# Kernel optimization log

Hardware: AMD Instinct MI355X
Metric: run time of the kernel (lower is better)

Reference implementation:

```python
import jax, jax.numpy as jnp
import numpy as np

B, T_IN, T_OUT, N, C, H, K1 = 4, 12, 24, 5000, 32, 8, 17  # K1 = k+1 (self included)
SIGMA_RATIO = 2.0
BETA = 0.8  # Swish beta
W_THRESH = 1e-5


def setup_inputs() -> dict:
    key = jax.random.key(0)
    k1, k2, k3, k4, k5 = jax.random.split(key, 5)
    x = jax.random.normal(k1, (B, T_IN, N, C), jnp.float32)
    nearest_nodes = jax.random.randint(k2, (N, K1), 0, N)  # int indices; -1 allowed by module semantics
    nearest_dists = jax.random.uniform(k3, (N, K1), jnp.float32) * 100.0
    W_shrink = jax.random.normal(k4, (T_IN * H, T_OUT - T_IN), jnp.float32) / np.float32(np.sqrt(T_IN * H))
    b_shrink = jax.random.normal(k5, (T_OUT - T_IN,), jnp.float32) * 0.01
    return {"x": x, "nearest_nodes": nearest_nodes, "nearest_dists": nearest_dists,
            "W_shrink": W_shrink, "b_shrink": b_shrink}


def reference(x, nearest_nodes, nearest_dists, W_shrink, b_shrink):
    Bx, t, n, c = x.shape
    sigma = nearest_dists.max() / SIGMA_RATIO
    lam = jnp.arange(1, H + 1, dtype=jnp.float32) / H  # (H,)
    nd = nearest_dists.reshape(-1)                      # (N*K1,)
    nn = nearest_nodes.reshape(-1)                      # (N*K1,)
    # GCN weights: exp(-d^2 * lambda / sigma^2), zeroed for missing (-1) neighbors and tiny values
    w = jnp.exp(-(nd[:, None] ** 2) * lam / (sigma ** 2))  # (N*K1, H)
    w = jnp.where(nn[:, None] == -1, 0.0, w)
    w = jnp.where(w < W_THRESH, 0.0, w)
    # pad row so index -1 hits zeros (jax -1 wraps to last row, matching torch)
    pad_x = jnp.concatenate([x, jnp.zeros((Bx, t, 1, c), x.dtype)], axis=2)
    x_nb = pad_x[:, :, nn].reshape(Bx, t, n, K1, c)         # gathered neighbors (B,t,N,K1,C)
    w3 = w.reshape(n, K1, H)
    # fused gather-weight-sum over neighbor dim j -> (B,t,N,H,C)
    agg = jnp.einsum('btnjc,njh->btnhc', x_nb, w3)
    # (B,t,N,H,C) -> (B,N,C,t,H) -> (B,N,C,t*H)
    feat = agg.transpose(0, 2, 4, 1, 3).reshape(Bx, n, c, t * H)
    y = feat @ W_shrink + b_shrink                          # (B,N,C,T-t_in)
    y = y.transpose(0, 3, 1, 2)                             # (B,T-t_in,N,C)
    y = y * jax.nn.sigmoid(BETA * y)                        # Swish
    return jnp.concatenate([x, y], axis=1)                  # (B,T,N,C)
```

## Files before the change

kernel.cpp:

```cpp
#include <hip/hip_runtime.h>

#define BB     4
#define T_IN   12
#define T_OUT  24
#define NNODES 5000
#define CC     32
#define HH     8
#define K1     17
#define O_OUT  12
#define XSTRIDE (NNODES*CC)
#define TPU     (NNODES*16)

#define XB2_BN  192
#define XB2_B   (NNODES*XB2_BN)
#define JP      9
#define VJPD    36
#define VQD     (JP*VJPD)
#define VND     (4*VQD)
#define PREPB   938

__global__ void max_reduce_kernel(const float* __restrict__ d, int n,
                                  unsigned* __restrict__ out) {
    float m = 0.0f;
    for (int i = blockIdx.x * blockDim.x + threadIdx.x; i < n;
         i += gridDim.x * blockDim.x)
        m = fmaxf(m, d[i]);
#pragma unroll
    for (int off = 32; off > 0; off >>= 1)
        m = fmaxf(m, __shfl_down(m, off, 64));
    if ((threadIdx.x & 63) == 0)
        atomicMax(out, __float_as_uint(m));
}

__device__ inline unsigned bf16rne(float f) {
    unsigned u = __float_as_uint(f);
    return (u + 0x7FFFu + ((u >> 16) & 1u)) >> 16;
}

__global__ void fused_prep_kernel(const float4* __restrict__ x,
                                  float4* __restrict__ out,
                                  uint4* __restrict__ xb2,
                                  const int* __restrict__ nn,
                                  const float* __restrict__ nd,
                                  const float* __restrict__ Wsh,
                                  const unsigned* __restrict__ maxbits,
                                  unsigned* __restrict__ Vb2) {
    __shared__ float wjl[144];
    const int tid = threadIdx.x;

    if (blockIdx.x < PREPB) {
        const int total = BB * T_IN * NNODES;
        for (int i = blockIdx.x * blockDim.x + tid; i < total;
             i += PREPB * blockDim.x) {
            int bt = i / NNODES;
            int n  = i - bt * NNODES;
            int b  = bt / T_IN;
            int t  = bt - b * T_IN;
            const float4* xr = x + (size_t)i * 8;
            float4* orow = out + ((size_t)(b * T_OUT + t) * NNODES + n) * 8;
            uint4* xrow  = xb2 + ((size_t)(b * NNODES + n) * T_IN + t) * 4;
#pragma unroll
            for (int vq = 0; vq < 4; ++vq) {
                float4 v0 = xr[2 * vq], v1 = xr[2 * vq + 1];
                orow[2 * vq] = v0; orow[2 * vq + 1] = v1;
                uint4 pk;
                pk.x = bf16rne(v0.x) | (bf16rne(v0.y) << 16);
                pk.y = bf16rne(v0.z) | (bf16rne(v0.w) << 16);
                pk.z = bf16rne(v1.x) | (bf16rne(v1.y) << 16);
                pk.w = bf16rne(v1.z) | (bf16rne(v1.w) << 16);
                xrow[vq] = pk;
            }
        }
    } else {
        const int n = blockIdx.x - PREPB;
        if (tid < 144) {
            int j = tid >> 3, h = tid & 7;
            float wv = 0.f;
            if (j < K1) {
                float mx = __uint_as_float(*maxbits);
                float inv_s2 = 4.0f / (mx * mx);
                float dv = nd[n * K1 + j];
                float lam = (float)(h + 1) * 0.125f;
                wv = expf(-dv * dv * lam * inv_s2);
                if (nn[n * K1 + j] == -1 || wv < 1e-5f) wv = 0.0f;
            }
            wjl[tid] = wv;
        }
        __syncthreads();
        if (tid < 144) {
            const int t = tid / 12;
            const int o = tid - t * 12;
            float Wcol[8];
#pragma unroll
            for (int h = 0; h < 8; ++h) Wcol[h] = Wsh[(t * 8 + h) * 12 + o];
            unsigned* vn = Vb2 + (size_t)n * VND
                         + (t / 3) * VQD + (t % 3) * 12 + o;
#pragma unroll
            for (int jp = 0; jp < JP; ++jp) {
                float4 a0 = *(const float4*)&wjl[jp * 16];
                float4 a1 = *(const float4*)&wjl[jp * 16 + 4];
                float4 b0 = *(const float4*)&wjl[jp * 16 + 8];
                float4 b1 = *(const float4*)&wjl[jp * 16 + 12];
                float wa[8] = {a0.x, a0.y, a0.z, a0.w, a1.x, a1.y, a1.z, a1.w};
                float wb[8] = {b0.x, b0.y, b0.z, b0.w, b1.x, b1.y, b1.z, b1.w};
                float v0 = 0.f, v1 = 0.f;
#pragma unroll
                for (int h = 0; h < 8; ++h) {
                    v0 = fmaf(wa[h], Wcol[h], v0);
                    v1 = fmaf(wb[h], Wcol[h], v1);
                }
                vn[jp * VJPD] = bf16rne(v0) | (bf16rne(v1) << 16);
            }
        }
    }
}

struct VBlk { uint4 v[9]; };

__device__ __forceinline__ unsigned u4c(const uint4& u, int i) {
    switch (i) { case 0: return u.x; case 1: return u.y;
                 case 2: return u.z; default: return u.w; }
}

#define DOT2(ACC, XP, VP) \
    asm("v_dot2_f32_bf16 %0, %1, %2, %0" : "+v"(ACC) : "v"(XP), "s"(VP))

__launch_bounds__(256)
__global__ void gnn_main5_kernel(const unsigned* __restrict__ xb2,
                                 const unsigned* __restrict__ Vb2,
                                 const int* __restrict__ nn,
                                 const float* __restrict__ bsh,
                                 float* __restrict__ out) {
    __shared__ float pb2[2][24][65];
    __shared__ float bl[O_OUT];

    const int n    = blockIdx.x;
    const int tid  = threadIdx.x;
    const int q    = __builtin_amdgcn_readfirstlane(tid >> 6);
    const int lane = tid & 63;
    const int bb   = lane >> 4;
    const int c2   = lane & 15;

    if (tid < O_OUT) bl[tid] = bsh[tid];

    int nnv[18];
#pragma unroll
    for (int j = 0; j < K1; ++j) nnv[j] = max(nn[n * K1 + j], 0);
    nnv[17] = nnv[16];

    const unsigned* xlane = xb2 + bb * XB2_B + 48 * q + c2;
    const unsigned* vbase = Vb2 + (size_t)n * VND + q * VQD;

    float pf[24];
#pragma unroll
    for (int i = 0; i < 24; ++i) pf[i] = 0.f;

#define VLOADP(DST, JPI) do {                                                \
        const uint4* vp_ = (const uint4*)(vbase + (JPI) * VJPD);             \
        _Pragma("unroll")                                                    \
        for (int i_ = 0; i_ < 9; ++i_) DST.v[i_] = vp_[i_];                  \
    } while (0)

#define XLOADP(E0, E1, E2, O0, O1, O2, JPI) do {                             \
        const unsigned* xe_ = xlane + nnv[2 * (JPI)] * XB2_BN;               \
        const unsigned* xo_ = xlane + nnv[2 * (JPI) + 1] * XB2_BN;           \
        E0 = xe_[0]; E1 = xe_[16]; E2 = xe_[32];                             \
        O0 = xo_[0]; O1 = xo_[16]; O2 = xo_[32];                             \
    } while (0)

#define COMPP(VV, E0, E1, E2, O0, O1, O2) do {                               \
        unsigned xe_[3] = {E0, E1, E2};                                      \
        unsigned xo_[3] = {O0, O1, O2};                                      \
        _Pragma("unroll")                                                    \
        for (int t_ = 0; t_ < 3; ++t_) {                                     \
            unsigned plo_ = __builtin_amdgcn_perm(xe_[t_], xo_[t_],          \
                                                  0x01000504u);              \
            unsigned phi_ = __builtin_amdgcn_perm(xe_[t_], xo_[t_],          \
                                                  0x03020706u);              \
            _Pragma("unroll")                                                \
            for (int o_ = 0; o_ < 12; ++o_) {                                \
                unsigned vp_ = u4c(VV.v[t_ * 3 + (o_ >> 2)], o_ & 3);        \
                DOT2(pf[o_],      plo_, vp_);                                \
                DOT2(pf[12 + o_], phi_, vp_);                                \
            }                                                                \
        }                                                                    \
    } while (0)

    VBlk va, vb;
    unsigned e00, e01, e02, o00, o01, o02;
    unsigned e10, e11, e12, o10, o11, o12;
    unsigned e20, e21, e22, o20, o21, o22;

    XLOADP(e00, e01, e02, o00, o01, o02, 0);
    XLOADP(e10, e11, e12, o10, o11, o12, 1);
    VLOADP(va, 0);
    VLOADP(vb, 1);
    XLOADP(e20, e21, e22, o20, o21, o22, 2);
    COMPP(va, e00, e01, e02, o00, o01, o02);
    VLOADP(va, 2);
    XLOADP(e00, e01, e02, o00, o01, o02, 3);
    COMPP(vb, e10, e11, e12, o10, o11, o12);
    VLOADP(vb, 3);
    XLOADP(e10, e11, e12, o10, o11, o12, 4);
    COMPP(va, e20, e21, e22, o20, o21, o22);
    VLOADP(va, 4);
    XLOADP(e20, e21, e22, o20, o21, o22, 5);
    COMPP(vb, e00, e01, e02, o00, o01, o02);
    VLOADP(vb, 5);
    XLOADP(e00, e01, e02, o00, o01, o02, 6);
    COMPP(va, e10, e11, e12, o10, o11, o12);
    VLOADP(va, 6);
    XLOADP(e10, e11, e12, o10, o11, o12, 7);
    COMPP(vb, e20, e21, e22, o20, o21, o22);
    VLOADP(vb, 7);
    XLOADP(e20, e21, e22, o20, o21, o22, 8);
    COMPP(va, e00, e01, e02, o00, o01, o02);
    VLOADP(va, 8);
    COMPP(vb, e10, e11, e12, o10, o11, o12);
    COMPP(va, e20, e21, e22, o20, o21, o22);

#undef VLOADP
#undef XLOADP
#undef COMPP

    if (q >= 2) {
#pragma unroll
        for (int i = 0; i < 24; ++i) pb2[q - 2][i][lane] = pf[i];
    }
    __syncthreads();
    if (q < 2) {
#pragma unroll
        for (int i = 0; i < 24; ++i) pf[i] += pb2[q][i][lane];
    }
    if (q == 1) {
#pragma unroll
        for (int i = 0; i < 24; ++i) pb2[1][i][lane] = pf[i];
    }
    __syncthreads();
    if (q == 0) {
        float* ob = out + ((size_t)(bb * T_OUT + T_IN) * NNODES + n) * CC + 2 * c2;
#pragma unroll
        for (int o = 0; o < O_OUT; ++o) {
            float v0 = pf[o]      + pb2[1][o][lane]      + bl[o];
            float v1 = pf[12 + o] + pb2[1][12 + o][lane] + bl[o];
            float s0 = v0 / (1.f + expf(-0.8f * v0));
            float s1 = v1 / (1.f + expf(-0.8f * v1));
            *(float2*)(ob + (size_t)o * XSTRIDE) = make_float2(s0, s1);
        }
    }
}

template <int PACK>
__global__ void prep_kernel(const float4* __restrict__ x,
                            float4* __restrict__ out,
                            uint2* __restrict__ xb) {
    const int PLANE4 = NNODES * CC / 4;
    const int total  = BB * T_IN * PLANE4;
    for (int i = blockIdx.x * blockDim.x + threadIdx.x; i < total;
         i += gridDim.x * blockDim.x) {
        int bt = i / PLANE4;
        int qq = i - bt * PLANE4;
        int b  = bt / T_IN;
        int t  = bt - b * T_IN;
        float4 v = x[i];
        out[((size_t)(b * T_OUT + t)) * PLANE4 + qq] = v;
        if (PACK) {
            uint2 pk;
            pk.x = bf16rne(v.x) | (bf16rne(v.y) << 16);
            pk.y = bf16rne(v.z) | (bf16rne(v.w) << 16);
            xb[i] = pk;
        }
    }
}

template <int USEBF>
__launch_bounds__(256)
__global__ void gnn_main_kernel(const float* __restrict__ x,
                                const unsigned* __restrict__ xbu,
                                const int* __restrict__ nn,
                                const float* __restrict__ nd,
                                const float* __restrict__ Wsh,
                                const float* __restrict__ bsh,
                                const unsigned* __restrict__ maxbits,
                                float* __restrict__ out) {
    __shared__ float wl[K1][HH];
    __shared__ float Wl[96][O_OUT];
    __shared__ float bl_s[O_OUT];
    __shared__ int   nnl[K1];

    const int n   = blockIdx.x;
    const int tid = threadIdx.x;
    const int rg  = tid >> 4;
    const int c2  = tid & 15;
    const int b   = rg >> 2;
    const int q   = rg & 3;

    for (int i = tid; i < 288; i += 256)
        ((float4*)Wl)[i] = ((const float4*)Wsh)[i];
    if (tid < O_OUT) bl_s[tid] = bsh[tid];
    if (tid < K1 * HH) {
        int j = tid >> 3, h = tid & 7;
        int v = nn[n * K1 + j];
        float dv = nd[n * K1 + j];
        float mx = __uint_as_float(*maxbits);
        float inv_s2 = 4.0f / (mx * mx);
        float lam = (float)(h + 1) * 0.125f;
        float wv = expf(-dv * dv * lam * inv_s2);
        if (v == -1 || wv < 1e-5f) wv = 0.0f;
        wl[j][h] = wv;
    }
    if (tid < K1) nnl[tid] = max(nn[n * K1 + tid], 0);
    __syncthreads();

    float acc[3][2][8];
#pragma unroll
    for (int k = 0; k < 3; ++k)
#pragma unroll
        for (int cc = 0; cc < 2; ++cc)
#pragma unroll
            for (int h = 0; h < 8; ++h) acc[k][cc][h] = 0.f;

    if (USEBF) {
        const unsigned* xbase = xbu + (b * T_IN + 3 * q) * TPU + c2;
        unsigned ua0, ua1, ua2, ub0, ub1, ub2;
#define LOADB(u0, u1, u2, J) do {                                            \
        int idx_ = __builtin_amdgcn_readfirstlane(nnl[(J)]);                 \
        const unsigned* bp_ = xbase + idx_ * 16;                             \
        u0 = bp_[0]; u1 = bp_[TPU]; u2 = bp_[2 * TPU];                       \
    } while (0)
#define COMPB(u0, u1, u2, J) do {                                            \
        float4 wA_ = *(const float4*)&wl[(J)][0];                            \
        float4 wB_ = *(const float4*)&wl[(J)][4];                            \
        float wv_[8] = {wA_.x, wA_.y, wA_.z, wA_.w,                          \
                        wB_.x, wB_.y, wB_.z, wB_.w};                         \
        float xl_[3] = {__uint_as_float(u0 << 16),                           \
                        __uint_as_float(u1 << 16),                           \
                        __uint_as_float(u2 << 16)};                          \
        float xh_[3] = {__uint_as_float(u0 & 0xffff0000u),                   \
                        __uint_as_float(u1 & 0xffff0000u),                   \
                        __uint_as_float(u2 & 0xffff0000u)};                  \
        _Pragma("unroll")                                                    \
        for (int k_ = 0; k_ < 3; ++k_)                                       \
            _Pragma("unroll")                                                \
            for (int h_ = 0; h_ < 8; ++h_) {                                 \
                acc[k_][0][h_] = fmaf(wv_[h_], xl_[k_], acc[k_][0][h_]);     \
                acc[k_][1][h_] = fmaf(wv_[h_], xh_[k_], acc[k_][1][h_]);     \
            }                                                                \
    } while (0)
        LOADB(ua0, ua1, ua2, 0);
#pragma unroll 1
        for (int jj = 0; jj < 8; ++jj) {
            LOADB(ub0, ub1, ub2, 2 * jj + 1);
            COMPB(ua0, ua1, ua2, 2 * jj);
            LOADB(ua0, ua1, ua2, 2 * jj + 2);
            COMPB(ub0, ub1, ub2, 2 * jj + 1);
        }
        COMPB(ua0, ua1, ua2, 16);
#undef LOADB
#undef COMPB
    } else {
        const float* xbase = x + (b * T_IN + 3 * q) * XSTRIDE + 2 * c2;
        float2 xa0, xa1, xa2, xb0, xb1, xb2;
#define LOADJ(v0, v1, v2, J) do {                                            \
        int idx_ = __builtin_amdgcn_readfirstlane(nnl[(J)]);                 \
        const float* bp_ = xbase + idx_ * CC;                                \
        v0 = *(const float2*)(bp_);                                          \
        v1 = *(const float2*)(bp_ + XSTRIDE);                                \
        v2 = *(const float2*)(bp_ + 2 * XSTRIDE);                            \
    } while (0)
#define COMPJ(v0, v1, v2, J) do {                                            \
        float4 wA_ = *(const float4*)&wl[(J)][0];                            \
        float4 wB_ = *(const float4*)&wl[(J)][4];                            \
        float wv_[8] = {wA_.x, wA_.y, wA_.z, wA_.w,                          \
                        wB_.x, wB_.y, wB_.z, wB_.w};                         \
        float xv_[3][2] = {{v0.x, v0.y}, {v1.x, v1.y}, {v2.x, v2.y}};        \
        _Pragma("unroll")                                                    \
        for (int k_ = 0; k_ < 3; ++k_)                                       \
            _Pragma("unroll")                                                \
            for (int cc_ = 0; cc_ < 2; ++cc_)                                \
                _Pragma("unroll")                                            \
                for (int h_ = 0; h_ < 8; ++h_)                               \
                    acc[k_][cc_][h_] =                                       \
                        fmaf(wv_[h_], xv_[k_][cc_], acc[k_][cc_][h_]);       \
    } while (0)
        LOADJ(xa0, xa1, xa2, 0);
#pragma unroll 1
        for (int jj = 0; jj < 8; ++jj) {
            LOADJ(xb0, xb1, xb2, 2 * jj + 1);
            COMPJ(xa0, xa1, xa2, 2 * jj);
            LOADJ(xa0, xa1, xa2, 2 * jj + 2);
            COMPJ(xb0, xb1, xb2, 2 * jj + 1);
        }
        COMPJ(xa0, xa1, xa2, 16);
#undef LOADJ
#undef COMPJ
    }

    float p[2][O_OUT];
#pragma unroll
    for (int o = 0; o < O_OUT; ++o) { p[0][o] = 0.f; p[1][o] = 0.f; }
#pragma unroll
    for (int k = 0; k < 3; ++k) {
#pragma unroll
        for (int h = 0; h < 8; ++h) {
            int row = (3 * q + k) * 8 + h;
            const float4* wr = (const float4*)&Wl[row][0];
            float4 w0 = wr[0], w1 = wr[1], w2 = wr[2];
            float wrow[12] = {w0.x, w0.y, w0.z, w0.w,
                              w1.x, w1.y, w1.z, w1.w,
                              w2.x, w2.y, w2.z, w2.w};
            float a0 = acc[k][0][h], a1 = acc[k][1][h];
#pragma unroll
            for (int o = 0; o < O_OUT; ++o) {
                p[0][o] = fmaf(a0, wrow[o], p[0][o]);
                p[1][o] = fmaf(a1, wrow[o], p[1][o]);
            }
        }
    }
#pragma unroll
    for (int cc = 0; cc < 2; ++cc)
#pragma unroll
        for (int o = 0; o < O_OUT; ++o) {
            float v = p[cc][o];
            v += __shfl_xor(v, 16, 64);
            v += __shfl_xor(v, 32, 64);
            p[cc][o] = v;
        }
    if (q == 0) {
        float* ob = out + ((size_t)(b * T_OUT + T_IN) * NNODES + n) * CC + 2 * c2;
#pragma unroll
        for (int o = 0; o < O_OUT; ++o) {
            float v0 = p[0][o] + bl_s[o];
            float v1 = p[1][o] + bl_s[o];
            float s0 = v0 / (1.f + expf(-0.8f * v0));
            float s1 = v1 / (1.f + expf(-0.8f * v1));
            *(float2*)(ob + (size_t)o * XSTRIDE) = make_float2(s0, s1);
        }
    }
}

extern "C" void kernel_launch(void* const* d_in, const int* in_sizes, int n_in,
                              void* d_out, int out_size, void* d_ws, size_t ws_size,
                              hipStream_t stream) {
    const float* x   = (const float*)d_in[0];
    const int*   nn  = (const int*)d_in[1];
    const float* nd  = (const float*)d_in[2];
    const float* Wsh = (const float*)d_in[3];
    const float* bsh = (const float*)d_in[4];
    float* out = (float*)d_out;

    unsigned* maxbits = (unsigned*)d_ws;
    hipMemsetAsync(d_ws, 0, sizeof(unsigned), stream);
    max_reduce_kernel<<<128, 256, 0, stream>>>(nd, NNODES * K1, maxbits);

    const size_t xb2_off = 1024;
    const size_t xb2_sz  = (size_t)BB * NNODES * T_IN * 16 * 4;
    const size_t vb_off  = xb2_off + xb2_sz;
    const size_t vb_sz   = (size_t)NNODES * VND * 4;
    const size_t need2   = vb_off + vb_sz;

    if (ws_size >= need2) {
        uint4*    xb2 = (uint4*)((char*)d_ws + xb2_off);
        unsigned* Vb2 = (unsigned*)((char*)d_ws + vb_off);

        fused_prep_kernel<<<PREPB + NNODES, 256, 0, stream>>>(
            (const float4*)x, (float4*)out, xb2, nn, nd, Wsh, maxbits, Vb2);
        gnn_main5_kernel<<<NNODES, 256, 0, stream>>>((const unsigned*)xb2, Vb2,
                                                     nn, bsh, out);
    } else {
        unsigned* xbu = (unsigned*)((char*)d_ws + 256);
        const size_t need1 = 256 + (size_t)BB * T_IN * NNODES * CC * 2;
        if (ws_size >= need1) {
            prep_kernel<1><<<2048, 256, 0, stream>>>((const float4*)x,
                                                     (float4*)out, (uint2*)xbu);
            gnn_main_kernel<1><<<NNODES, 256, 0, stream>>>(x, xbu, nn, nd, Wsh,
                                                           bsh, maxbits, out);
        } else {
            prep_kernel<0><<<2048, 256, 0, stream>>>((const float4*)x,
                                                     (float4*)out, (uint2*)xbu);
            gnn_main_kernel<0><<<NNODES, 256, 0, stream>>>(x, xbu, nn, nd, Wsh,
                                                           bsh, maxbits, out);
        }
    }
}
```

Before: 90.52 us.

## Interleave batch into node-major bf16 layout and preload all neighbor gathers

The bf16 copy of x is reorganized so that all four batches of a node sit contiguously (node, t, batch, c), which turns each neighbor gather into one contiguous 3 KB region instead of four scattered ones. The main kernel also issues all 9 pairs of neighbor loads up front into registers rather than software-pipelining them alongside the V loads. This is meant to improve cache-line and DRAM locality of the gather and to expose more memory-level parallelism. In exchange it holds 54 extra live registers, which may reduce occupancy.

```diff
diff --git a/kernel.cpp b/kernel.cpp
--- a/kernel.cpp
+++ b/kernel.cpp
@@ -11,8 +11,7 @@
 #define XSTRIDE (NNODES*CC)
 #define TPU     (NNODES*16)
 
-#define XB2_BN  192
-#define XB2_B   (NNODES*XB2_BN)
+#define XB3_N   768
 #define JP      9
 #define VJPD    36
 #define VQD     (JP*VJPD)
@@ -39,7 +38,7 @@
 
 __global__ void fused_prep_kernel(const float4* __restrict__ x,
                                   float4* __restrict__ out,
-                                  uint4* __restrict__ xb2,
+                                  uint4* __restrict__ xb3,
                                   const int* __restrict__ nn,
                                   const float* __restrict__ nd,
                                   const float* __restrict__ Wsh,
@@ -58,7 +57,7 @@
             int t  = bt - b * T_IN;
             const float4* xr = x + (size_t)i * 8;
             float4* orow = out + ((size_t)(b * T_OUT + t) * NNODES + n) * 8;
-            uint4* xrow  = xb2 + ((size_t)(b * NNODES + n) * T_IN + t) * 4;
+            uint4* xrow = xb3 + ((size_t)((n * T_IN + t) * 4 + b)) * 4;
 #pragma unroll
             for (int vq = 0; vq < 4; ++vq) {
                 float4 v0 = xr[2 * vq], v1 = xr[2 * vq + 1];
@@ -126,7 +125,7 @@
     asm("v_dot2_f32_bf16 %0, %1, %2, %0" : "+v"(ACC) : "v"(XP), "s"(VP))
 
 __launch_bounds__(256)
-__global__ void gnn_main5_kernel(const unsigned* __restrict__ xb2,
+__global__ void gnn_main6_kernel(const unsigned* __restrict__ xb3,
                                  const unsigned* __restrict__ Vb2,
                                  const int* __restrict__ nn,
                                  const float* __restrict__ bsh,
@@ -148,12 +147,21 @@
     for (int j = 0; j < K1; ++j) nnv[j] = max(nn[n * K1 + j], 0);
     nnv[17] = nnv[16];
 
-    const unsigned* xlane = xb2 + bb * XB2_B + 48 * q + c2;
+    const unsigned* xlane = xb3 + (3 * q) * 64 + bb * 16 + c2;
     const unsigned* vbase = Vb2 + (size_t)n * VND + q * VQD;
 
     float pf[24];
 #pragma unroll
     for (int i = 0; i < 24; ++i) pf[i] = 0.f;
+
+    unsigned XE[9][3], XO[9][3];
+#pragma unroll
+    for (int jp = 0; jp < 9; ++jp) {
+        const unsigned* xe_ = xlane + nnv[2 * jp]     * XB3_N;
+        const unsigned* xo_ = xlane + nnv[2 * jp + 1] * XB3_N;
+        XE[jp][0] = xe_[0]; XE[jp][1] = xe_[64]; XE[jp][2] = xe_[128];
+        XO[jp][0] = xo_[0]; XO[jp][1] = xo_[64]; XO[jp][2] = xo_[128];
+    }
 
 #define VLOADP(DST, JPI) do {                                                \
         const uint4* vp_ = (const uint4*)(vbase + (JPI) * VJPD);             \
@@ -161,21 +169,12 @@
         for (int i_ = 0; i_ < 9; ++i_) DST.v[i_] = vp_[i_];                  \
     } while (0)
 
-#define XLOADP(E0, E1, E2, O0, O1, O2, JPI) do {                             \
-        const unsigned* xe_ = xlane + nnv[2 * (JPI)] * XB2_BN;               \
-        const unsigned* xo_ = xlane + nnv[2 * (JPI) + 1] * XB2_BN;           \
-        E0 = xe_[0]; E1 = xe_[16]; E2 = xe_[32];                             \
-        O0 = xo_[0]; O1 = xo_[16]; O2 = xo_[32];                             \
-    } while (0)
-
-#define COMPP(VV, E0, E1, E2, O0, O1, O2) do {                               \
-        unsigned xe_[3] = {E0, E1, E2};                                      \
-        unsigned xo_[3] = {O0, O1, O2};                                      \
+#define COMPP(VV, JPI) do {                                                  \
         _Pragma("unroll")                                                    \
         for (int t_ = 0; t_ < 3; ++t_) {                                     \
-            unsigned plo_ = __builtin_amdgcn_perm(xe_[t_], xo_[t_],          \
+            unsigned plo_ = __builtin_amdgcn_perm(XE[JPI][t_], XO[JPI][t_],  \
                                                   0x01000504u);              \
-            unsigned phi_ = __builtin_amdgcn_perm(xe_[t_], xo_[t_],          \
+            unsigned phi_ = __builtin_amdgcn_perm(XE[JPI][t_], XO[JPI][t_],  \
                                                   0x03020706u);              \
             _Pragma("unroll")                                                \
             for (int o_ = 0; o_ < 12; ++o_) {                                \
@@ -187,40 +186,19 @@
     } while (0)
 
     VBlk va, vb;
-    unsigned e00, e01, e02, o00, o01, o02;
-    unsigned e10, e11, e12, o10, o11, o12;
-    unsigned e20, e21, e22, o20, o21, o22;
-
-    XLOADP(e00, e01, e02, o00, o01, o02, 0);
-    XLOADP(e10, e11, e12, o10, o11, o12, 1);
     VLOADP(va, 0);
     VLOADP(vb, 1);
-    XLOADP(e20, e21, e22, o20, o21, o22, 2);
-    COMPP(va, e00, e01, e02, o00, o01, o02);
-    VLOADP(va, 2);
-    XLOADP(e00, e01, e02, o00, o01, o02, 3);
-    COMPP(vb, e10, e11, e12, o10, o11, o12);
-    VLOADP(vb, 3);
-    XLOADP(e10, e11, e12, o10, o11, o12, 4);
-    COMPP(va, e20, e21, e22, o20, o21, o22);
-    VLOADP(va, 4);
-    XLOADP(e20, e21, e22, o20, o21, o22, 5);
-    COMPP(vb, e00, e01, e02, o00, o01, o02);
-    VLOADP(vb, 5);
-    XLOADP(e00, e01, e02, o00, o01, o02, 6);
-    COMPP(va, e10, e11, e12, o10, o11, o12);
-    VLOADP(va, 6);
-    XLOADP(e10, e11, e12, o10, o11, o12, 7);
-    COMPP(vb, e20, e21, e22, o20, o21, o22);
-    VLOADP(vb, 7);
-    XLOADP(e20, e21, e22, o20, o21, o22, 8);
-    COMPP(va, e00, e01, e02, o00, o01, o02);
-    VLOADP(va, 8);
-    COMPP(vb, e10, e11, e12, o10, o11, o12);
-    COMPP(va, e20, e21, e22, o20, o21, o22);
+    COMPP(va, 0); VLOADP(va, 2);
+    COMPP(vb, 1); VLOADP(vb, 3);
+    COMPP(va, 2); VLOADP(va, 4);
+    COMPP(vb, 3); VLOADP(vb, 5);
+    COMPP(va, 4); VLOADP(va, 6);
+    COMPP(vb, 5); VLOADP(vb, 7);
+    COMPP(va, 6); VLOADP(va, 8);
+    COMPP(vb, 7);
+    COMPP(va, 8);
 
 #undef VLOADP
-#undef XLOADP
 #undef COMPP
 
     if (q >= 2) {
@@ -453,19 +431,19 @@
     hipMemsetAsync(d_ws, 0, sizeof(unsigned), stream);
     max_reduce_kernel<<<128, 256, 0, stream>>>(nd, NNODES * K1, maxbits);
 
-    const size_t xb2_off = 1024;
-    const size_t xb2_sz  = (size_t)BB * NNODES * T_IN * 16 * 4;
-    const size_t vb_off  = xb2_off + xb2_sz;
+    const size_t xb3_off = 1024;
+    const size_t xb3_sz  = (size_t)NNODES * XB3_N * 4;
+    const size_t vb_off  = xb3_off + xb3_sz;
     const size_t vb_sz   = (size_t)NNODES * VND * 4;
     const size_t need2   = vb_off + vb_sz;
 
     if (ws_size >= need2) {
-        uint4*    xb2 = (uint4*)((char*)d_ws + xb2_off);
+        uint4*    xb3 = (uint4*)((char*)d_ws + xb3_off);
         unsigned* Vb2 = (unsigned*)((char*)d_ws + vb_off);
 
         fused_prep_kernel<<<PREPB + NNODES, 256, 0, stream>>>(
-            (const float4*)x, (float4*)out, xb2, nn, nd, Wsh, maxbits, Vb2);
-        gnn_main5_kernel<<<NNODES, 256, 0, stream>>>((const unsigned*)xb2, Vb2,
+            (const float4*)x, (float4*)out, xb3, nn, nd, Wsh, maxbits, Vb2);
+        gnn_main6_kernel<<<NNODES, 256, 0, stream>>>((const unsigned*)xb3, Vb2,
                                                      nn, bsh, out);
     } else {
         unsigned* xbu = (unsigned*)((char*)d_ws + 256);
```

After: 92.60 us. +2.3%, slower.

## Build per-node V projections in LDS inside main kernel instead of global prep

Applied to the files above, without the earlier changes.

The prep kernel now only computes the per-node Gaussian weight table (17x8 floats) and the x copy/bf16 pack in a uniform grid-stride kernel. The main kernel loads the weight row plus W_shrink and computes the bf16-packed V matrix into LDS, then reads V from LDS instead of global memory. This is meant to remove the larger global V buffer write and read round trip. In exchange the main kernel does extra FMA work and a block barrier before compute, and the dot instruction operand changes from SGPR to VGPR.

```diff
diff --git a/kernel.cpp b/kernel.cpp
--- a/kernel.cpp
+++ b/kernel.cpp
@@ -17,7 +17,7 @@
 #define VJPD    36
 #define VQD     (JP*VJPD)
 #define VND     (4*VQD)
-#define PREPB   938
+#define WJN     144
 
 __global__ void max_reduce_kernel(const float* __restrict__ d, int n,
                                   unsigned* __restrict__ out) {
@@ -37,81 +37,53 @@
     return (u + 0x7FFFu + ((u >> 16) & 1u)) >> 16;
 }
 
-__global__ void fused_prep_kernel(const float4* __restrict__ x,
-                                  float4* __restrict__ out,
-                                  uint4* __restrict__ xb2,
-                                  const int* __restrict__ nn,
-                                  const float* __restrict__ nd,
-                                  const float* __restrict__ Wsh,
-                                  const unsigned* __restrict__ maxbits,
-                                  unsigned* __restrict__ Vb2) {
-    __shared__ float wjl[144];
-    const int tid = threadIdx.x;
-
-    if (blockIdx.x < PREPB) {
-        const int total = BB * T_IN * NNODES;
-        for (int i = blockIdx.x * blockDim.x + tid; i < total;
-             i += PREPB * blockDim.x) {
-            int bt = i / NNODES;
-            int n  = i - bt * NNODES;
-            int b  = bt / T_IN;
-            int t  = bt - b * T_IN;
-            const float4* xr = x + (size_t)i * 8;
-            float4* orow = out + ((size_t)(b * T_OUT + t) * NNODES + n) * 8;
-            uint4* xrow  = xb2 + ((size_t)(b * NNODES + n) * T_IN + t) * 4;
-#pragma unroll
-            for (int vq = 0; vq < 4; ++vq) {
-                float4 v0 = xr[2 * vq], v1 = xr[2 * vq + 1];
-                orow[2 * vq] = v0; orow[2 * vq + 1] = v1;
-                uint4 pk;
-                pk.x = bf16rne(v0.x) | (bf16rne(v0.y) << 16);
-                pk.y = bf16rne(v0.z) | (bf16rne(v0.w) << 16);
-                pk.z = bf16rne(v1.x) | (bf16rne(v1.y) << 16);
-                pk.w = bf16rne(v1.z) | (bf16rne(v1.w) << 16);
-                xrow[vq] = pk;
-            }
-        }
-    } else {
-        const int n = blockIdx.x - PREPB;
-        if (tid < 144) {
-            int j = tid >> 3, h = tid & 7;
-            float wv = 0.f;
-            if (j < K1) {
-                float mx = __uint_as_float(*maxbits);
-                float inv_s2 = 4.0f / (mx * mx);
-                float dv = nd[n * K1 + j];
-                float lam = (float)(h + 1) * 0.125f;
-                wv = expf(-dv * dv * lam * inv_s2);
-                if (nn[n * K1 + j] == -1 || wv < 1e-5f) wv = 0.0f;
-            }
-            wjl[tid] = wv;
-        }
-        __syncthreads();
-        if (tid < 144) {
-            const int t = tid / 12;
-            const int o = tid - t * 12;
-            float Wcol[8];
-#pragma unroll
-            for (int h = 0; h < 8; ++h) Wcol[h] = Wsh[(t * 8 + h) * 12 + o];
-            unsigned* vn = Vb2 + (size_t)n * VND
-                         + (t / 3) * VQD + (t % 3) * 12 + o;
-#pragma unroll
-            for (int jp = 0; jp < JP; ++jp) {
-                float4 a0 = *(const float4*)&wjl[jp * 16];
-                float4 a1 = *(const float4*)&wjl[jp * 16 + 4];
-                float4 b0 = *(const float4*)&wjl[jp * 16 + 8];
-                float4 b1 = *(const float4*)&wjl[jp * 16 + 12];
-                float wa[8] = {a0.x, a0.y, a0.z, a0.w, a1.x, a1.y, a1.z, a1.w};
-                float wb[8] = {b0.x, b0.y, b0.z, b0.w, b1.x, b1.y, b1.z, b1.w};
-                float v0 = 0.f, v1 = 0.f;
-#pragma unroll
-                for (int h = 0; h < 8; ++h) {
-                    v0 = fmaf(wa[h], Wcol[h], v0);
-                    v1 = fmaf(wb[h], Wcol[h], v1);
-                }
-                vn[jp * VJPD] = bf16rne(v0) | (bf16rne(v1) << 16);
-            }
-        }
+__global__ void prep4_kernel(const float4* __restrict__ x,
+                             float4* __restrict__ out,
+                             uint4* __restrict__ xb2,
+                             const int* __restrict__ nn,
+                             const float* __restrict__ nd,
+                             const unsigned* __restrict__ maxbits,
+                             float* __restrict__ wjg) {
+    const int gs = gridDim.x * blockDim.x;
+    const int g0 = blockIdx.x * blockDim.x + threadIdx.x;
+
+    const int totalA = BB * T_IN * NNODES;
+    for (int i = g0; i < totalA; i += gs) {
+        int bt = i / NNODES;
+        int nd_ = i - bt * NNODES;
+        int b  = bt / T_IN;
+        int t  = bt - b * T_IN;
+        const float4* xr = x + (size_t)i * 8;
+        float4* orow = out + ((size_t)(b * T_OUT + t) * NNODES + nd_) * 8;
+        uint4* xrow  = xb2 + ((size_t)(b * NNODES + nd_) * T_IN + t) * 4;
+#pragma unroll
+        for (int vq = 0; vq < 4; ++vq) {
+            float4 v0 = xr[2 * vq], v1 = xr[2 * vq + 1];
+            orow[2 * vq] = v0; orow[2 * vq + 1] = v1;
+            uint4 pk;
+            pk.x = bf16rne(v0.x) | (bf16rne(v0.y) << 16);
+            pk.y = bf16rne(v0.z) | (bf16rne(v0.w) << 16);
+            pk.z = bf16rne(v1.x) | (bf16rne(v1.y) << 16);
+            pk.w = bf16rne(v1.z) | (bf16rne(v1.w) << 16);
+            xrow[vq] = pk;
+        }
+    }
+
+    float mx = __uint_as_float(*maxbits);
+    float inv_s2 = 4.0f / (mx * mx);
+    const int totalB = NNODES * WJN;
+    for (int i = g0; i < totalB; i += gs) {
+        int n = i / WJN;
+        int r = i - n * WJN;
+        int j = r >> 3, h = r & 7;
+        float wv = 0.f;
+        if (j < K1) {
+            float dv = nd[n * K1 + j];
+            float lam = (float)(h + 1) * 0.125f;
+            wv = expf(-dv * dv * lam * inv_s2);
+            if (nn[n * K1 + j] == -1 || wv < 1e-5f) wv = 0.0f;
+        }
+        wjg[i] = wv;
     }
 }
 
@@ -123,15 +95,17 @@
 }
 
 #define DOT2(ACC, XP, VP) \
-    asm("v_dot2_f32_bf16 %0, %1, %2, %0" : "+v"(ACC) : "v"(XP), "s"(VP))
+    asm("v_dot2_f32_bf16 %0, %1, %2, %0" : "+v"(ACC) : "v"(XP), "v"(VP))
 
 __launch_bounds__(256)
-__global__ void gnn_main5_kernel(const unsigned* __restrict__ xb2,
-                                 const unsigned* __restrict__ Vb2,
+__global__ void gnn_main7_kernel(const unsigned* __restrict__ xb2,
+                                 const float* __restrict__ wjg,
+                                 const float* __restrict__ Wsh,
                                  const int* __restrict__ nn,
                                  const float* __restrict__ bsh,
                                  float* __restrict__ out) {
     __shared__ float pb2[2][24][65];
+    __shared__ unsigned Vl[VND];
     __shared__ float bl[O_OUT];
 
     const int n    = blockIdx.x;
@@ -149,23 +123,58 @@
     nnv[17] = nnv[16];
 
     const unsigned* xlane = xb2 + bb * XB2_B + 48 * q + c2;
-    const unsigned* vbase = Vb2 + (size_t)n * VND + q * VQD;
-
-    float pf[24];
-#pragma unroll
-    for (int i = 0; i < 24; ++i) pf[i] = 0.f;
-
-#define VLOADP(DST, JPI) do {                                                \
-        const uint4* vp_ = (const uint4*)(vbase + (JPI) * VJPD);             \
-        _Pragma("unroll")                                                    \
-        for (int i_ = 0; i_ < 9; ++i_) DST.v[i_] = vp_[i_];                  \
-    } while (0)
 
 #define XLOADP(E0, E1, E2, O0, O1, O2, JPI) do {                             \
         const unsigned* xe_ = xlane + nnv[2 * (JPI)] * XB2_BN;               \
         const unsigned* xo_ = xlane + nnv[2 * (JPI) + 1] * XB2_BN;           \
         E0 = xe_[0]; E1 = xe_[16]; E2 = xe_[32];                             \
         O0 = xo_[0]; O1 = xo_[16]; O2 = xo_[32];                             \
+    } while (0)
+
+    unsigned e00, e01, e02, o00, o01, o02;
+    unsigned e10, e11, e12, o10, o11, o12;
+    unsigned e20, e21, e22, o20, o21, o22;
+
+    XLOADP(e00, e01, e02, o00, o01, o02, 0);
+    XLOADP(e10, e11, e12, o10, o11, o12, 1);
+
+    {
+        const int t = tid / 12;
+        const int o = tid - t * 12;
+        float Wcol[8];
+        if (tid < 144) {
+#pragma unroll
+            for (int h = 0; h < 8; ++h) Wcol[h] = Wsh[(t * 8 + h) * 12 + o];
+        }
+        const float* wp = wjg + n * WJN;
+        const int vi = (t / 3) * VQD + (t % 3) * 12 + o;
+#pragma unroll
+        for (int jp = 0; jp < JP; ++jp) {
+            float wa[16];
+#pragma unroll
+            for (int h = 0; h < 16; ++h) wa[h] = wp[jp * 16 + h];
+            if (tid < 144) {
+                float v0 = 0.f, v1 = 0.f;
+#pragma unroll
+                for (int h = 0; h < 8; ++h) {
+                    v0 = fmaf(wa[h],     Wcol[h], v0);
+                    v1 = fmaf(wa[8 + h], Wcol[h], v1);
+                }
+                Vl[vi + jp * VJPD] = bf16rne(v0) | (bf16rne(v1) << 16);
+            }
+        }
+    }
+
+    float pf[24];
+#pragma unroll
+    for (int i = 0; i < 24; ++i) pf[i] = 0.f;
+
+    __syncthreads();
+
+#define VLOADP(DST, JPI) do {                                                \
+        const uint4* vp_ = (const uint4*)&Vl[q * VQD + (JPI) * VJPD];        \
+        _Pragma("unroll")                                                    \
+        for (int i_ = 0; i_ < 9; ++i_) DST.v[i_] = vp_[i_];                  \
     } while (0)
 
 #define COMPP(VV, E0, E1, E2, O0, O1, O2) do {                               \
@@ -187,12 +196,6 @@
     } while (0)
 
     VBlk va, vb;
-    unsigned e00, e01, e02, o00, o01, o02;
-    unsigned e10, e11, e12, o10, o11, o12;
-    unsigned e20, e21, e22, o20, o21, o22;
-
-    XLOADP(e00, e01, e02, o00, o01, o02, 0);
-    XLOADP(e10, e11, e12, o10, o11, o12, 1);
     VLOADP(va, 0);
     VLOADP(vb, 1);
     XLOADP(e20, e21, e22, o20, o21, o22, 2);
@@ -453,20 +456,20 @@
     hipMemsetAsync(d_ws, 0, sizeof(unsigned), stream);
     max_reduce_kernel<<<128, 256, 0, stream>>>(nd, NNODES * K1, maxbits);
 
-    const size_t xb2_off = 1024;
+    const size_t wjg_off = 1024;
+    const size_t wjg_sz  = (size_t)NNODES * WJN * 4;
+    const size_t xb2_off = wjg_off + wjg_sz;
     const size_t xb2_sz  = (size_t)BB * NNODES * T_IN * 16 * 4;
-    const size_t vb_off  = xb2_off + xb2_sz;
-    const size_t vb_sz   = (size_t)NNODES * VND * 4;
-    const size_t need2   = vb_off + vb_sz;
+    const size_t need2   = xb2_off + xb2_sz;
 
     if (ws_size >= need2) {
-        uint4*    xb2 = (uint4*)((char*)d_ws + xb2_off);
-        unsigned* Vb2 = (unsigned*)((char*)d_ws + vb_off);
-
-        fused_prep_kernel<<<PREPB + NNODES, 256, 0, stream>>>(
-            (const float4*)x, (float4*)out, xb2, nn, nd, Wsh, maxbits, Vb2);
-        gnn_main5_kernel<<<NNODES, 256, 0, stream>>>((const unsigned*)xb2, Vb2,
-                                                     nn, bsh, out);
+        float* wjg = (float*)((char*)d_ws + wjg_off);
+        uint4* xb2 = (uint4*)((char*)d_ws + xb2_off);
+
+        prep4_kernel<<<2048, 256, 0, stream>>>(
+            (const float4*)x, (float4*)out, xb2, nn, nd, maxbits, wjg);
+        gnn_main7_kernel<<<NNODES, 256, 0, stream>>>(
+            (const unsigned*)xb2, wjg, Wsh, nn, bsh, out);
     } else {
         unsigned* xbu = (unsigned*)((char*)d_ws + 256);
         const size_t need1 = 256 + (size_t)BB * T_IN * NNODES * CC * 2;
```

Result: faster. 86.42 us (-4.5%).

## Restructure prep pipeline: fuse max-reduce into copy, split V build, plane-major bf16 x

Applied to the files above, without the earlier changes.

Folds the max-distance reduction into a grid-stride copy/convert kernel and moves the per-node V-matrix build into its own kernel, so the V build waits on the full max instead of sharing a launch with it. The bf16 copy of x now keeps the original (b,t,n,c) plane-major order instead of node-major, which makes the conversion a straight coalesced streaming pass. The main kernel's neighbour gather then reads three separate time planes per neighbour instead of one contiguous 192-word row, which may cost gather locality. This adds one kernel launch but removes the separate max-reduce launch.

```diff
diff --git a/kernel.cpp b/kernel.cpp
--- a/kernel.cpp
+++ b/kernel.cpp
@@ -11,13 +11,10 @@
 #define XSTRIDE (NNODES*CC)
 #define TPU     (NNODES*16)
 
-#define XB2_BN  192
-#define XB2_B   (NNODES*XB2_BN)
 #define JP      9
 #define VJPD    36
 #define VQD     (JP*VJPD)
 #define VND     (4*VQD)
-#define PREPB   938
 
 __global__ void max_reduce_kernel(const float* __restrict__ d, int n,
                                   unsigned* __restrict__ out) {
@@ -37,80 +34,84 @@
     return (u + 0x7FFFu + ((u >> 16) & 1u)) >> 16;
 }
 
-__global__ void fused_prep_kernel(const float4* __restrict__ x,
-                                  float4* __restrict__ out,
-                                  uint4* __restrict__ xb2,
-                                  const int* __restrict__ nn,
-                                  const float* __restrict__ nd,
-                                  const float* __restrict__ Wsh,
-                                  const unsigned* __restrict__ maxbits,
-                                  unsigned* __restrict__ Vb2) {
+__global__ void prep5b_kernel(const float4* __restrict__ x,
+                              float4* __restrict__ out,
+                              uint2* __restrict__ xbu,
+                              const float* __restrict__ nd,
+                              unsigned* __restrict__ maxbits) {
+    const int gs = gridDim.x * blockDim.x;
+    const int g0 = blockIdx.x * blockDim.x + threadIdx.x;
+
+    {
+        float m = 0.0f;
+        for (int i = g0; i < NNODES * K1; i += gs) m = fmaxf(m, nd[i]);
+#pragma unroll
+        for (int off = 32; off > 0; off >>= 1)
+            m = fmaxf(m, __shfl_down(m, off, 64));
+        if ((threadIdx.x & 63) == 0 && m > 0.0f)
+            atomicMax(maxbits, __float_as_uint(m));
+    }
+
+    const int PLANE4 = NNODES * CC / 4;
+    const int total  = BB * T_IN * PLANE4;
+    for (int i = g0; i < total; i += gs) {
+        int bt = i / PLANE4;
+        int qq = i - bt * PLANE4;
+        int b  = bt / T_IN;
+        int t  = bt - b * T_IN;
+        float4 v = x[i];
+        out[((size_t)(b * T_OUT + t)) * PLANE4 + qq] = v;
+        uint2 pk;
+        pk.x = bf16rne(v.x) | (bf16rne(v.y) << 16);
+        pk.y = bf16rne(v.z) | (bf16rne(v.w) << 16);
+        xbu[i] = pk;
+    }
+}
+
+__launch_bounds__(192)
+__global__ void vbuild4_kernel(const int* __restrict__ nn,
+                               const float* __restrict__ nd,
+                               const float* __restrict__ Wsh,
+                               const unsigned* __restrict__ maxbits,
+                               unsigned* __restrict__ Vb2) {
     __shared__ float wjl[144];
-    const int tid = threadIdx.x;
-
-    if (blockIdx.x < PREPB) {
-        const int total = BB * T_IN * NNODES;
-        for (int i = blockIdx.x * blockDim.x + tid; i < total;
-             i += PREPB * blockDim.x) {
-            int bt = i / NNODES;
-            int n  = i - bt * NNODES;
-            int b  = bt / T_IN;
-            int t  = bt - b * T_IN;
-            const float4* xr = x + (size_t)i * 8;
-            float4* orow = out + ((size_t)(b * T_OUT + t) * NNODES + n) * 8;
-            uint4* xrow  = xb2 + ((size_t)(b * NNODES + n) * T_IN + t) * 4;
-#pragma unroll
-            for (int vq = 0; vq < 4; ++vq) {
-                float4 v0 = xr[2 * vq], v1 = xr[2 * vq + 1];
-                orow[2 * vq] = v0; orow[2 * vq + 1] = v1;
-                uint4 pk;
-                pk.x = bf16rne(v0.x) | (bf16rne(v0.y) << 16);
-                pk.y = bf16rne(v0.z) | (bf16rne(v0.w) << 16);
-                pk.z = bf16rne(v1.x) | (bf16rne(v1.y) << 16);
-                pk.w = bf16rne(v1.z) | (bf16rne(v1.w) << 16);
-                xrow[vq] = pk;
+    const int n = blockIdx.x, tid = threadIdx.x;
+    if (tid < 144) {
+        int j = tid >> 3, h = tid & 7;
+        float wv = 0.f;
+        if (j < K1) {
+            float mx = __uint_as_float(*maxbits);
+            float inv_s2 = 4.0f / (mx * mx);
+            float dv = nd[n * K1 + j];
+            float lam = (float)(h + 1) * 0.125f;
+            wv = expf(-dv * dv * lam * inv_s2);
+            if (nn[n * K1 + j] == -1 || wv < 1e-5f) wv = 0.0f;
+        }
+        wjl[tid] = wv;
+    }
+    __syncthreads();
+    if (tid < 144) {
+        const int t = tid / 12;
+        const int o = tid - t * 12;
+        float Wcol[8];
+#pragma unroll
+        for (int h = 0; h < 8; ++h) Wcol[h] = Wsh[(t * 8 + h) * 12 + o];
+        unsigned* vn = Vb2 + (size_t)n * VND + (t / 3) * VQD + (t % 3) * 12 + o;
+#pragma unroll
+        for (int jp = 0; jp < JP; ++jp) {
+            float4 a0 = *(const float4*)&wjl[jp * 16];
+            float4 a1 = *(const float4*)&wjl[jp * 16 + 4];
+            float4 b0 = *(const float4*)&wjl[jp * 16 + 8];
+            float4 b1 = *(const float4*)&wjl[jp * 16 + 12];
+            float wa[8] = {a0.x, a0.y, a0.z, a0.w, a1.x, a1.y, a1.z, a1.w};
+            float wb[8] = {b0.x, b0.y, b0.z, b0.w, b1.x, b1.y, b1.z, b1.w};
+            float v0 = 0.f, v1 = 0.f;
+#pragma unroll
+            for (int h = 0; h < 8; ++h) {
+                v0 = fmaf(wa[h], Wcol[h], v0);
+                v1 = fmaf(wb[h], Wcol[h], v1);
             }
-        }
-    } else {
-        const int n = blockIdx.x - PREPB;
-        if (tid < 144) {
-            int j = tid >> 3, h = tid & 7;
-            float wv = 0.f;
-            if (j < K1) {
-                float mx = __uint_as_float(*maxbits);
-                float inv_s2 = 4.0f / (mx * mx);
-                float dv = nd[n * K1 + j];
-                float lam = (float)(h + 1) * 0.125f;
-                wv = expf(-dv * dv * lam * inv_s2);
-                if (nn[n * K1 + j] == -1 || wv < 1e-5f) wv = 0.0f;
-            }
-            wjl[tid] = wv;
-        }
-        __syncthreads();
-        if (tid < 144) {
-            const int t = tid / 12;
-            const int o = tid - t * 12;
-            float Wcol[8];
-#pragma unroll
-            for (int h = 0; h < 8; ++h) Wcol[h] = Wsh[(t * 8 + h) * 12 + o];
-            unsigned* vn = Vb2 + (size_t)n * VND
-                         + (t / 3) * VQD + (t % 3) * 12 + o;
-#pragma unroll
-            for (int jp = 0; jp < JP; ++jp) {
-                float4 a0 = *(const float4*)&wjl[jp * 16];
-                float4 a1 = *(const float4*)&wjl[jp * 16 + 4];
-                float4 b0 = *(const float4*)&wjl[jp * 16 + 8];
-                float4 b1 = *(const float4*)&wjl[jp * 16 + 12];
-                float wa[8] = {a0.x, a0.y, a0.z, a0.w, a1.x, a1.y, a1.z, a1.w};
-                float wb[8] = {b0.x, b0.y, b0.z, b0.w, b1.x, b1.y, b1.z, b1.w};
-                float v0 = 0.f, v1 = 0.f;
-#pragma unroll
-                for (int h = 0; h < 8; ++h) {
-                    v0 = fmaf(wa[h], Wcol[h], v0);
-                    v1 = fmaf(wb[h], Wcol[h], v1);
-                }
-                vn[jp * VJPD] = bf16rne(v0) | (bf16rne(v1) << 16);
-            }
+            vn[jp * VJPD] = bf16rne(v0) | (bf16rne(v1) << 16);
         }
     }
 }
@@ -126,11 +127,11 @@
     asm("v_dot2_f32_bf16 %0, %1, %2, %0" : "+v"(ACC) : "v"(XP), "s"(VP))
 
 __launch_bounds__(256)
-__global__ void gnn_main5_kernel(const unsigned* __restrict__ xb2,
-                                 const unsigned* __restrict__ Vb2,
-                                 const int* __restrict__ nn,
-                                 const float* __restrict__ bsh,
-                                 float* __restrict__ out) {
+__global__ void gnn_main11_kernel(const unsigned* __restrict__ xbu,
+                                  const unsigned* __restrict__ Vb2,
+                                  const int* __restrict__ nn,
+                                  const float* __restrict__ bsh,
+                                  float* __restrict__ out) {
     __shared__ float pb2[2][24][65];
     __shared__ float bl[O_OUT];
 
@@ -148,7 +149,7 @@
     for (int j = 0; j < K1; ++j) nnv[j] = max(nn[n * K1 + j], 0);
     nnv[17] = nnv[16];
 
-    const unsigned* xlane = xb2 + bb * XB2_B + 48 * q + c2;
+    const unsigned* xlane = xbu + (bb * T_IN + 3 * q) * TPU + c2;
     const unsigned* vbase = Vb2 + (size_t)n * VND + q * VQD;
 
     float pf[24];
@@ -162,10 +163,10 @@
     } while (0)
 
 #define XLOADP(E0, E1, E2, O0, O1, O2, JPI) do {                             \
-        const unsigned* xe_ = xlane + nnv[2 * (JPI)] * XB2_BN;               \
-        const unsigned* xo_ = xlane + nnv[2 * (JPI) + 1] * XB2_BN;           \
-        E0 = xe_[0]; E1 = xe_[16]; E2 = xe_[32];                             \
-        O0 = xo_[0]; O1 = xo_[16]; O2 = xo_[32];                             \
+        const unsigned* xe_ = xlane + nnv[2 * (JPI)] * 16;                   \
+        const unsigned* xo_ = xlane + nnv[2 * (JPI) + 1] * 16;               \
+        E0 = xe_[0]; E1 = xe_[TPU]; E2 = xe_[2 * TPU];                       \
+        O0 = xo_[0]; O1 = xo_[TPU]; O2 = xo_[2 * TPU];                       \
     } while (0)
 
 #define COMPP(VV, E0, E1, E2, O0, O1, O2) do {                               \
@@ -451,23 +452,24 @@
 
     unsigned* maxbits = (unsigned*)d_ws;
     hipMemsetAsync(d_ws, 0, sizeof(unsigned), stream);
-    max_reduce_kernel<<<128, 256, 0, stream>>>(nd, NNODES * K1, maxbits);
-
-    const size_t xb2_off = 1024;
-    const size_t xb2_sz  = (size_t)BB * NNODES * T_IN * 16 * 4;
-    const size_t vb_off  = xb2_off + xb2_sz;
+
+    const size_t xbu_off = 1024;
+    const size_t xbu_sz  = (size_t)BB * T_IN * NNODES * CC * 2;
+    const size_t vb_off  = xbu_off + xbu_sz;
     const size_t vb_sz   = (size_t)NNODES * VND * 4;
     const size_t need2   = vb_off + vb_sz;
 
     if (ws_size >= need2) {
-        uint4*    xb2 = (uint4*)((char*)d_ws + xb2_off);
+        uint2*    xbu = (uint2*)((char*)d_ws + xbu_off);
         unsigned* Vb2 = (unsigned*)((char*)d_ws + vb_off);
 
-        fused_prep_kernel<<<PREPB + NNODES, 256, 0, stream>>>(
-            (const float4*)x, (float4*)out, xb2, nn, nd, Wsh, maxbits, Vb2);
-        gnn_main5_kernel<<<NNODES, 256, 0, stream>>>((const unsigned*)xb2, Vb2,
-                                                     nn, bsh, out);
+        prep5b_kernel<<<2048, 256, 0, stream>>>(
+            (const float4*)x, (float4*)out, xbu, nd, maxbits);
+        vbuild4_kernel<<<NNODES, 192, 0, stream>>>(nn, nd, Wsh, maxbits, Vb2);
+        gnn_main11_kernel<<<NNODES, 256, 0, stream>>>(
+            (const unsigned*)xbu, Vb2, nn, bsh, out);
     } else {
+        max_reduce_kernel<<<128, 256, 0, stream>>>(nd, NNODES * K1, maxbits);
         unsigned* xbu = (unsigned*)((char*)d_ws + 256);
         const size_t need1 = 256 + (size_t)BB * T_IN * NNODES * CC * 2;
         if (ws_size >= need1) {
```

Measured after the change: 115.1 us. 1.27x slower.
